# Optimization experiments

Measured on AMD Instinct MI355X. Metric: run time of the kernel, lower is better.

## Reference

```python
import jax, jax.numpy as jnp
import numpy as np

N, C_IN, H, W = 32, 256, 56, 56
C_OUT, KH, KW = 256, 3, 3
ACT_BITS = 8


def setup_inputs() -> dict:
    key = jax.random.key(0)
    k_x, k_w, k_s, k_b = jax.random.split(key, 4)
    x = jax.random.normal(k_x, (N, C_IN, H, W), dtype=jnp.float32)
    # ternary weights in {-1, 0, +1}, stored as int8
    w_q = jax.random.randint(k_w, (C_OUT, C_IN, KH, KW), -1, 2).astype(jnp.int8)
    # per-output-channel scale, broadcastable over NCHW as [C,1,1]
    s = (jax.random.uniform(k_s, (C_OUT, 1, 1), dtype=jnp.float32) * 0.02 + 0.005)
    bias = jax.random.normal(k_b, (C_OUT,), dtype=jnp.float32) * 0.1
    act_s = jnp.float32(1.0 / 127.0)  # per-tensor activation quant scale
    return {"x": x, "w_q": w_q, "s": s, "bias": bias, "act_s": act_s}


def reference(x, w_q, s, bias, act_s):
    # activation fake-quant: clamp to [-1,1], round to act_bits symmetric grid
    qmax = (1 << (ACT_BITS - 1)) - 1  # 127
    x = jnp.clip(x, -1.0, 1.0)
    x_int = jnp.clip(jnp.round(x / act_s), -qmax, qmax)
    xq = x_int * act_s
    # ternary conv (weights upcast to float), stride 1, pad 1, dilation 1
    y = jax.lax.conv_general_dilated(
        xq, w_q.astype(jnp.float32),
        window_strides=(1, 1), padding=((1, 1), (1, 1)),
        lhs_dilation=(1, 1), rhs_dilation=(1, 1),
        dimension_numbers=("NCHW", "OIHW", "NCHW"), feature_group_count=1)
    # per-output-channel scale + bias
    y = y * s + bias.reshape(1, -1, 1, 1)
    return y
```

## Files before the change

kernel.cpp:

```cpp
#include <hip/hip_runtime.h>

typedef int v4i __attribute__((ext_vector_type(4)));

#define NIMG 32
#define CIN  256
#define COUT 256
#define HW   3136
#define W56  56
#define HP   58
#define PIMG (HP * HP)
#define XQP_BYTES (NIMG * PIMG * CIN)
#define WP_BYTES  (9 * COUT * CIN)

#define BARRIER() asm volatile("s_barrier" ::: "memory")
#define VMCNT(n)  asm volatile("s_waitcnt vmcnt(" #n ")" ::: "memory")

__global__ __launch_bounds__(256) void zero_border(v4i* __restrict__ p)
{
    int i = blockIdx.x * 256 + threadIdx.x;
    if (i >= NIMG * 228 * 16) return;
    int n = i / 3648, r = i % 3648, pix = r >> 4, c = r & 15;
    int h, w;
    if (pix < 58)       { h = 0;         w = pix;       }
    else if (pix < 116) { h = 57;        w = pix - 58;  }
    else if (pix < 172) { h = pix - 115; w = 0;         }
    else                { h = pix - 171; w = 57;        }
    v4i z = {0, 0, 0, 0};
    p[(size_t)(n * PIMG + h * HP + w) * 16 + c] = z;
}

__global__ __launch_bounds__(256) void quantize_pad(
    const float* __restrict__ x, signed char* __restrict__ xqp)
{
    __shared__ int tile[64][65];
    const int n  = blockIdx.z;
    const int c0 = blockIdx.y * 64;
    const int p0 = blockIdx.x * 64;
    const int tid = threadIdx.x;

    const int px   = tid & 63;
    const int crow = tid >> 6;
    const float* xb = x + ((size_t)(n * CIN + c0)) * HW + p0;
#pragma unroll
    for (int i = 0; i < 16; ++i) {
        int c = crow + i * 4;
        float v = xb[(size_t)c * HW + px];
        v = fminf(fmaxf(v, -1.f), 1.f);
        tile[c][px] = (int)rintf(v * 127.f);
    }
    __syncthreads();

    const int c4   = tid & 15;
    const int prow = tid >> 4;
#pragma unroll
    for (int i = 0; i < 4; ++i) {
        int p  = prow + i * 16;
        int hw = p0 + p;
        int oh = hw / W56, ow = hw % W56;
        int b0 = tile[c4 * 4 + 0][p] & 255;
        int b1 = tile[c4 * 4 + 1][p] & 255;
        int b2 = tile[c4 * 4 + 2][p] & 255;
        int b3 = tile[c4 * 4 + 3][p] & 255;
        int packed = b0 | (b1 << 8) | (b2 << 16) | (b3 << 24);
        *(int*)(xqp + ((size_t)(n * PIMG + (oh + 1) * HP + (ow + 1))) * CIN
                    + c0 + c4 * 4) = packed;
    }
}

__global__ __launch_bounds__(256) void repack_w(
    const int* __restrict__ wq, signed char* __restrict__ wp2)
{
    int idx  = blockIdx.x * 256 + threadIdx.x;
    int t    = idx >> 16;
    int rem  = idx & 65535;
    int kc   = rem >> 14;
    int rem2 = rem & 16383;
    int co   = rem2 >> 6;
    int c6   = rem2 & 63;
    int ci   = kc * 64 + c6;
    wp2[idx] = (signed char)wq[(co * CIN + ci) * 9 + t];
}

__device__ __forceinline__ void gll16(const void* g, void* l)
{
    __builtin_amdgcn_global_load_lds(
        (const __attribute__((address_space(1))) int*)g,
        (__attribute__((address_space(3))) int*)l, 16, 0, 0);
}

__global__ __launch_bounds__(256) void bitconv_mfma(
    const signed char* __restrict__ xqp, const signed char* __restrict__ wp2,
    const float* __restrict__ s_, const float* __restrict__ bias,
    const float* __restrict__ act_s_p, float* __restrict__ out)
{
    __shared__ signed char lds[3][16384];

    const int tid  = threadIdx.x;
    const int lane = tid & 63;
    const int wid  = tid >> 6;
    const int wr   = wid >> 1;
    const int wc   = wid & 1;
    const int l15  = lane & 15;
    const int kg   = lane >> 4;
    const int kgs  = ((kg ^ ((l15 >> 1) & 3)) << 4);

    const int b  = blockIdx.x;
    const int w  = (b & 7) * 196 + (b >> 3);
    const int px0   = (w >> 1) * 128;
    const int cout0 = (w & 1) * 128;

    const int srow   = tid >> 2;
    const int schunk = (((tid & 3) ^ ((tid >> 3) & 3)) << 4);
    const signed char* asrc = wp2 + cout0 * 64 + srow * 64 + schunk;

    const signed char* bsrc[2];
#pragma unroll
    for (int r = 0; r < 2; ++r) {
        int p = px0 + srow + r * 64;
        int n = p / HW, q = p % HW;
        bsrc[r] = xqp
            + ((size_t)(n * PIMG + (q / W56 + 1) * HP + (q % W56 + 1))) * CIN
            + schunk;
    }

    int aoff[4], boff[4];
#pragma unroll
    for (int i = 0; i < 4; ++i)
        aoff[i] = (wr * 64 + i * 16 + l15) * 64 + kgs;
#pragma unroll
    for (int j = 0; j < 4; ++j)
        boff[j] = 8192 + (wc * 64 + j * 16 + l15) * 64 + kgs;

    v4i acc[4][4] = {};

    const int wb = wid * 1024;

    auto stage = [&](int buf, int s) {
        int t9 = s >> 2, kc = s & 3;
        int bo = ((t9 / 3 - 1) * HP + (t9 % 3 - 1)) * CIN + kc * 64;
        signed char* L = &lds[buf][0];
        const signed char* a = asrc + s * 16384;
        gll16(a,            L + wb);
        gll16(a + 4096,     L + 4096  + wb);
        gll16(bsrc[0] + bo, L + 8192  + wb);
        gll16(bsrc[1] + bo, L + 12288 + wb);
    };

    stage(0, 0);
    stage(1, 1);
    VMCNT(4);
    BARRIER();

    for (int it = 0; it < 12; ++it) {
#pragma unroll
        for (int u = 0; u < 3; ++u) {
            const int s = it * 3 + u;
            const signed char* L = &lds[u][0];

            if (s <= 33) stage((u + 2) % 3, s + 2);

            v4i a[4], bb[4];
#pragma unroll
            for (int i = 0; i < 4; ++i) a[i]  = *(const v4i*)(L + aoff[i]);
#pragma unroll
            for (int j = 0; j < 4; ++j) bb[j] = *(const v4i*)(L + boff[j]);

            BARRIER();
            __builtin_amdgcn_s_setprio(1);
#pragma unroll
            for (int i = 0; i < 2; ++i)
#pragma unroll
                for (int j = 0; j < 4; ++j)
                    acc[i][j] = __builtin_amdgcn_mfma_i32_16x16x64_i8(
                        a[i], bb[j], acc[i][j], 0, 0, 0);
            __builtin_amdgcn_s_setprio(0);

            BARRIER();
            __builtin_amdgcn_s_setprio(1);
#pragma unroll
            for (int i = 2; i < 4; ++i)
#pragma unroll
                for (int j = 0; j < 4; ++j)
                    acc[i][j] = __builtin_amdgcn_mfma_i32_16x16x64_i8(
                        a[i], bb[j], acc[i][j], 0, 0, 0);
            __builtin_amdgcn_s_setprio(0);

            if (s <= 33)      { VMCNT(4); }
            else if (s == 34) { VMCNT(0); }
            if (s < 35) BARRIER();
        }
    }

    const float a_s = act_s_p[0];
    int nn[4], hh[4];
#pragma unroll
    for (int j = 0; j < 4; ++j) {
        int op = px0 + wc * 64 + j * 16 + l15;
        nn[j] = op / HW;
        hh[j] = op % HW;
    }
#pragma unroll
    for (int i = 0; i < 4; ++i) {
        int cb = cout0 + wr * 64 + i * 16 + kg * 4;
        float sc[4], bi[4];
#pragma unroll
        for (int r = 0; r < 4; ++r) {
            sc[r] = a_s * s_[cb + r];
            bi[r] = bias[cb + r];
        }
#pragma unroll
        for (int j = 0; j < 4; ++j)
#pragma unroll
            for (int r = 0; r < 4; ++r)
                out[((size_t)(nn[j] * COUT + cb + r)) * HW + hh[j]] =
                    (float)acc[i][j][r] * sc[r] + bi[r];
    }
}

extern "C" void kernel_launch(void* const* d_in, const int* in_sizes, int n_in,
                              void* d_out, int out_size, void* d_ws, size_t ws_size,
                              hipStream_t stream)
{
    const float* x     = (const float*)d_in[0];
    const int*   w_q   = (const int*)d_in[1];
    const float* s     = (const float*)d_in[2];
    const float* bias  = (const float*)d_in[3];
    const float* act_s = (const float*)d_in[4];

    signed char* xqp = (signed char*)d_ws;
    signed char* wp2 = (signed char*)d_ws + XQP_BYTES;

    zero_border<<<(NIMG * 228 * 16 + 255) / 256, 256, 0, stream>>>((v4i*)xqp);
    quantize_pad<<<dim3(49, 4, NIMG), 256, 0, stream>>>(x, xqp);
    repack_w<<<dim3(WP_BYTES / 256), 256, 0, stream>>>(w_q, wp2);
    bitconv_mfma<<<dim3(1568), 256, 0, stream>>>(
        xqp, wp2, s, bias, act_s, (float*)d_out);
}
```

Baseline: 99.34 us.

## Enlarge conv block tile to all 256 output channels, halving grid

Each block now computes 128 pixels by all 256 output channels instead of 128x128, so activation tiles are loaded once per pixel block rather than twice. The grid drops from 1568 to 784 blocks, LDS per stage grows to 24KB, and the accumulator array doubles to 8x4. Weight and activation loads are split into separate staging calls interleaved between the two MFMA halves. This raises register pressure (launch bounds request 2 blocks per CU) and reduces the number of blocks available to spread across CUs.

```diff
diff --git a/kernel.cpp b/kernel.cpp
--- a/kernel.cpp
+++ b/kernel.cpp
@@ -88,12 +88,12 @@
         (__attribute__((address_space(3))) int*)l, 16, 0, 0);
 }
 
-__global__ __launch_bounds__(256) void bitconv_mfma(
+__global__ __launch_bounds__(256, 2) void bitconv_mfma(
     const signed char* __restrict__ xqp, const signed char* __restrict__ wp2,
     const float* __restrict__ s_, const float* __restrict__ bias,
     const float* __restrict__ act_s_p, float* __restrict__ out)
 {
-    __shared__ signed char lds[3][16384];
+    __shared__ signed char lds[3][24576];
 
     const int tid  = threadIdx.x;
     const int lane = tid & 63;
@@ -104,14 +104,12 @@
     const int kg   = lane >> 4;
     const int kgs  = ((kg ^ ((l15 >> 1) & 3)) << 4);
 
-    const int b  = blockIdx.x;
-    const int w  = (b & 7) * 196 + (b >> 3);
-    const int px0   = (w >> 1) * 128;
-    const int cout0 = (w & 1) * 128;
+    const int b   = blockIdx.x;
+    const int px0 = ((b & 7) * 98 + (b >> 3)) * 128;
 
     const int srow   = tid >> 2;
     const int schunk = (((tid & 3) ^ ((tid >> 3) & 3)) << 4);
-    const signed char* asrc = wp2 + cout0 * 64 + srow * 64 + schunk;
+    const signed char* asrc = wp2 + srow * 64 + schunk;
 
     const signed char* bsrc[2];
 #pragma unroll
@@ -123,69 +121,81 @@
             + schunk;
     }
 
-    int aoff[4], boff[4];
-#pragma unroll
-    for (int i = 0; i < 4; ++i)
-        aoff[i] = (wr * 64 + i * 16 + l15) * 64 + kgs;
+    int aoff[8], boff[4];
+#pragma unroll
+    for (int i = 0; i < 8; ++i)
+        aoff[i] = (wr * 128 + i * 16 + l15) * 64 + kgs;
 #pragma unroll
     for (int j = 0; j < 4; ++j)
-        boff[j] = 8192 + (wc * 64 + j * 16 + l15) * 64 + kgs;
-
-    v4i acc[4][4] = {};
+        boff[j] = 16384 + (wc * 64 + j * 16 + l15) * 64 + kgs;
+
+    v4i acc[8][4] = {};
 
     const int wb = wid * 1024;
 
-    auto stage = [&](int buf, int s) {
+    auto stageA = [&](int buf, int s) {
+        signed char* L = &lds[buf][0];
+        const signed char* a = asrc + s * 16384;
+#pragma unroll
+        for (int k = 0; k < 4; ++k)
+            gll16(a + k * 4096, L + k * 4096 + wb);
+    };
+    auto stageB = [&](int buf, int s) {
         int t9 = s >> 2, kc = s & 3;
         int bo = ((t9 / 3 - 1) * HP + (t9 % 3 - 1)) * CIN + kc * 64;
         signed char* L = &lds[buf][0];
-        const signed char* a = asrc + s * 16384;
-        gll16(a,            L + wb);
-        gll16(a + 4096,     L + 4096  + wb);
-        gll16(bsrc[0] + bo, L + 8192  + wb);
-        gll16(bsrc[1] + bo, L + 12288 + wb);
+        gll16(bsrc[0] + bo, L + 16384 + wb);
+        gll16(bsrc[1] + bo, L + 20480 + wb);
     };
 
-    stage(0, 0);
-    stage(1, 1);
-    VMCNT(4);
+    stageA(0, 0); stageB(0, 0);
+    stageA(1, 1); stageB(1, 1);
+    VMCNT(6);
     BARRIER();
 
     for (int it = 0; it < 12; ++it) {
 #pragma unroll
         for (int u = 0; u < 3; ++u) {
             const int s = it * 3 + u;
+            const int nb = (u + 2) % 3;
             const signed char* L = &lds[u][0];
 
-            if (s <= 33) stage((u + 2) % 3, s + 2);
-
             v4i a[4], bb[4];
 #pragma unroll
+            for (int j = 0; j < 4; ++j) bb[j] = *(const v4i*)(L + boff[j]);
+#pragma unroll
             for (int i = 0; i < 4; ++i) a[i]  = *(const v4i*)(L + aoff[i]);
-#pragma unroll
-            for (int j = 0; j < 4; ++j) bb[j] = *(const v4i*)(L + boff[j]);
+
+            if (s <= 33) stageA(nb, s + 2);
 
             BARRIER();
             __builtin_amdgcn_s_setprio(1);
 #pragma unroll
-            for (int i = 0; i < 2; ++i)
+            for (int i = 0; i < 4; ++i)
 #pragma unroll
                 for (int j = 0; j < 4; ++j)
                     acc[i][j] = __builtin_amdgcn_mfma_i32_16x16x64_i8(
                         a[i], bb[j], acc[i][j], 0, 0, 0);
             __builtin_amdgcn_s_setprio(0);
+            BARRIER();
+
+            v4i a2[4];
+#pragma unroll
+            for (int i = 0; i < 4; ++i) a2[i] = *(const v4i*)(L + aoff[4 + i]);
+
+            if (s <= 33) stageB(nb, s + 2);
 
             BARRIER();
             __builtin_amdgcn_s_setprio(1);
 #pragma unroll
-            for (int i = 2; i < 4; ++i)
+            for (int i = 0; i < 4; ++i)
 #pragma unroll
                 for (int j = 0; j < 4; ++j)
-                    acc[i][j] = __builtin_amdgcn_mfma_i32_16x16x64_i8(
-                        a[i], bb[j], acc[i][j], 0, 0, 0);
+                    acc[4 + i][j] = __builtin_amdgcn_mfma_i32_16x16x64_i8(
+                        a2[i], bb[j], acc[4 + i][j], 0, 0, 0);
             __builtin_amdgcn_s_setprio(0);
 
-            if (s <= 33)      { VMCNT(4); }
+            if (s <= 33)      { VMCNT(6); }
             else if (s == 34) { VMCNT(0); }
             if (s < 35) BARRIER();
         }
@@ -200,8 +210,8 @@
         hh[j] = op % HW;
     }
 #pragma unroll
-    for (int i = 0; i < 4; ++i) {
-        int cb = cout0 + wr * 64 + i * 16 + kg * 4;
+    for (int i = 0; i < 8; ++i) {
+        int cb = wr * 128 + i * 16 + kg * 4;
         float sc[4], bi[4];
 #pragma unroll
         for (int r = 0; r < 4; ++r) {
@@ -233,6 +243,6 @@
     zero_border<<<(NIMG * 228 * 16 + 255) / 256, 256, 0, stream>>>((v4i*)xqp);
     quantize_pad<<<dim3(49, 4, NIMG), 256, 0, stream>>>(x, xqp);
     repack_w<<<dim3(WP_BYTES / 256), 256, 0, stream>>>(w_q, wp2);
-    bitconv_mfma<<<dim3(1568), 256, 0, stream>>>(
+    bitconv_mfma<<<dim3(784), 256, 0, stream>>>(
         xqp, wp2, s, bias, act_s, (float*)d_out);
 }
```

New measurement: 98.71 us. No clear change (-0.6%).

## Load weight fragments directly to registers and quad-buffer activations in LDS

Applied to the files above, without the earlier changes.

Weight (A) tiles are no longer staged through LDS. Each wave now loads its A fragments straight from global memory into registers, with a one-step register prefetch (a_cur/a_nxt). Only the activation (B) tile goes through LDS, which now uses a 4-deep ring of 8KB buffers, and the pipeline collapses to a single barrier per K step. This is meant to cut LDS traffic and barrier count, at the cost of uncoalesced-per-wave global loads for weights, more VGPRs for the prefetched A, and redundant A reads across the two waves sharing a row.

```diff
diff --git a/kernel.cpp b/kernel.cpp
--- a/kernel.cpp
+++ b/kernel.cpp
@@ -93,7 +93,7 @@
     const float* __restrict__ s_, const float* __restrict__ bias,
     const float* __restrict__ act_s_p, float* __restrict__ out)
 {
-    __shared__ signed char lds[3][16384];
+    __shared__ signed char Bs[4][8192];
 
     const int tid  = threadIdx.x;
     const int lane = tid & 63;
@@ -111,8 +111,6 @@
 
     const int srow   = tid >> 2;
     const int schunk = (((tid & 3) ^ ((tid >> 3) & 3)) << 4);
-    const signed char* asrc = wp2 + cout0 * 64 + srow * 64 + schunk;
-
     const signed char* bsrc[2];
 #pragma unroll
     for (int r = 0; r < 2; ++r) {
@@ -123,72 +121,63 @@
             + schunk;
     }
 
-    int aoff[4], boff[4];
-#pragma unroll
-    for (int i = 0; i < 4; ++i)
-        aoff[i] = (wr * 64 + i * 16 + l15) * 64 + kgs;
+    const signed char* ap = wp2 + (cout0 + wr * 64 + l15) * 64 + kg * 16;
+
+    int boff[4];
 #pragma unroll
     for (int j = 0; j < 4; ++j)
-        boff[j] = 8192 + (wc * 64 + j * 16 + l15) * 64 + kgs;
+        boff[j] = (wc * 64 + j * 16 + l15) * 64 + kgs;
 
     v4i acc[4][4] = {};
+    v4i a_cur[4], a_nxt[4];
 
     const int wb = wid * 1024;
 
-    auto stage = [&](int buf, int s) {
+    auto stageB = [&](int buf, int s) {
         int t9 = s >> 2, kc = s & 3;
         int bo = ((t9 / 3 - 1) * HP + (t9 % 3 - 1)) * CIN + kc * 64;
-        signed char* L = &lds[buf][0];
-        const signed char* a = asrc + s * 16384;
-        gll16(a,            L + wb);
-        gll16(a + 4096,     L + 4096  + wb);
-        gll16(bsrc[0] + bo, L + 8192  + wb);
-        gll16(bsrc[1] + bo, L + 12288 + wb);
+        signed char* L = &Bs[buf][0];
+        gll16(bsrc[0] + bo, L + wb);
+        gll16(bsrc[1] + bo, L + 4096 + wb);
     };
 
-    stage(0, 0);
-    stage(1, 1);
-    VMCNT(4);
-    BARRIER();
-
-    for (int it = 0; it < 12; ++it) {
-#pragma unroll
-        for (int u = 0; u < 3; ++u) {
-            const int s = it * 3 + u;
-            const signed char* L = &lds[u][0];
-
-            if (s <= 33) stage((u + 2) % 3, s + 2);
-
-            v4i a[4], bb[4];
-#pragma unroll
-            for (int i = 0; i < 4; ++i) a[i]  = *(const v4i*)(L + aoff[i]);
-#pragma unroll
-            for (int j = 0; j < 4; ++j) bb[j] = *(const v4i*)(L + boff[j]);
-
-            BARRIER();
-            __builtin_amdgcn_s_setprio(1);
-#pragma unroll
-            for (int i = 0; i < 2; ++i)
-#pragma unroll
-                for (int j = 0; j < 4; ++j)
-                    acc[i][j] = __builtin_amdgcn_mfma_i32_16x16x64_i8(
-                        a[i], bb[j], acc[i][j], 0, 0, 0);
-            __builtin_amdgcn_s_setprio(0);
-
-            BARRIER();
-            __builtin_amdgcn_s_setprio(1);
-#pragma unroll
-            for (int i = 2; i < 4; ++i)
-#pragma unroll
-                for (int j = 0; j < 4; ++j)
-                    acc[i][j] = __builtin_amdgcn_mfma_i32_16x16x64_i8(
-                        a[i], bb[j], acc[i][j], 0, 0, 0);
-            __builtin_amdgcn_s_setprio(0);
-
-            if (s <= 33)      { VMCNT(4); }
-            else if (s == 34) { VMCNT(0); }
-            if (s < 35) BARRIER();
+    stageB(0, 0);
+    stageB(1, 1);
+#pragma unroll
+    for (int i = 0; i < 4; ++i)
+        a_cur[i] = *(const v4i*)(ap + i * 1024);
+
+    for (int s = 0; s < 36; ++s) {
+        if (s < 35) {
+            const signed char* a = ap + (s + 1) * 16384;
+#pragma unroll
+            for (int i = 0; i < 4; ++i)
+                a_nxt[i] = *(const v4i*)(a + i * 1024);
         }
+        if (s < 34) stageB((s + 2) & 3, s + 2);
+
+        if (s == 0)       { VMCNT(6); }
+        else if (s <= 33) { VMCNT(8); }
+        else if (s == 34) { VMCNT(6); }
+        else              { VMCNT(0); }
+        BARRIER();
+
+        const signed char* L = &Bs[s & 3][0];
+        v4i bb[4];
+#pragma unroll
+        for (int j = 0; j < 4; ++j) bb[j] = *(const v4i*)(L + boff[j]);
+
+        __builtin_amdgcn_s_setprio(1);
+#pragma unroll
+        for (int i = 0; i < 4; ++i)
+#pragma unroll
+            for (int j = 0; j < 4; ++j)
+                acc[i][j] = __builtin_amdgcn_mfma_i32_16x16x64_i8(
+                    a_cur[i], bb[j], acc[i][j], 0, 0, 0);
+        __builtin_amdgcn_s_setprio(0);
+
+#pragma unroll
+        for (int i = 0; i < 4; ++i) a_cur[i] = a_nxt[i];
     }
 
     const float a_s = act_s_p[0];
```

After: 115.6 us. +16.4%, slower.

## Switch to double-buffered K=128 stages with one barrier per stage

Applied to the files above, without the earlier changes.

Replaces the triple-buffered 64-wide K pipeline with a double buffer where each stage loads two K=64 slices (32KB per buffer) and waits on vmcnt(0) once per stage. The intermediate barriers between MFMA halves are removed, so each stage now has one barrier instead of three. In exchange, prefetch depth drops to a single stage ahead and each wait drains all outstanding loads, which exposes more load latency. LDS use grows from 48KB to 64KB per block, which can lower occupancy.

```diff
diff --git a/kernel.cpp b/kernel.cpp
--- a/kernel.cpp
+++ b/kernel.cpp
@@ -13,7 +13,7 @@
 #define WP_BYTES  (9 * COUT * CIN)
 
 #define BARRIER() asm volatile("s_barrier" ::: "memory")
-#define VMCNT(n)  asm volatile("s_waitcnt vmcnt(" #n ")" ::: "memory")
+#define VMCNT0()  asm volatile("s_waitcnt vmcnt(0)" ::: "memory")
 
 __global__ __launch_bounds__(256) void zero_border(v4i* __restrict__ p)
 {
@@ -88,12 +88,18 @@
         (__attribute__((address_space(3))) int*)l, 16, 0, 0);
 }
 
+__device__ __forceinline__ int boffset(int ss)
+{
+    int t9 = ss >> 2, kc = ss & 3;
+    return ((t9 / 3 - 1) * HP + (t9 % 3 - 1)) * CIN + kc * 64;
+}
+
 __global__ __launch_bounds__(256) void bitconv_mfma(
     const signed char* __restrict__ xqp, const signed char* __restrict__ wp2,
     const float* __restrict__ s_, const float* __restrict__ bias,
     const float* __restrict__ act_s_p, float* __restrict__ out)
 {
-    __shared__ signed char lds[3][16384];
+    __shared__ signed char lds[2][32768];
 
     const int tid  = threadIdx.x;
     const int lane = tid & 63;
@@ -135,29 +141,32 @@
 
     const int wb = wid * 1024;
 
-    auto stage = [&](int buf, int s) {
-        int t9 = s >> 2, kc = s & 3;
-        int bo = ((t9 / 3 - 1) * HP + (t9 % 3 - 1)) * CIN + kc * 64;
+    auto stage = [&](int buf, int t) {
         signed char* L = &lds[buf][0];
-        const signed char* a = asrc + s * 16384;
-        gll16(a,            L + wb);
-        gll16(a + 4096,     L + 4096  + wb);
-        gll16(bsrc[0] + bo, L + 8192  + wb);
-        gll16(bsrc[1] + bo, L + 12288 + wb);
+#pragma unroll
+        for (int h = 0; h < 2; ++h) {
+            const int ss = 2 * t + h;
+            const signed char* a = asrc + ss * 16384;
+            const int R = h * 16384;
+            gll16(a,        L + R + wb);
+            gll16(a + 4096, L + R + 4096 + wb);
+            int bo = boffset(ss);
+            gll16(bsrc[0] + bo, L + R + 8192  + wb);
+            gll16(bsrc[1] + bo, L + R + 12288 + wb);
+        }
     };
 
     stage(0, 0);
-    stage(1, 1);
-    VMCNT(4);
+    VMCNT0();
     BARRIER();
 
-    for (int it = 0; it < 12; ++it) {
-#pragma unroll
-        for (int u = 0; u < 3; ++u) {
-            const int s = it * 3 + u;
+    for (int it = 0; it < 9; ++it) {
+#pragma unroll
+        for (int u = 0; u < 2; ++u) {
+            const int t = it * 2 + u;
             const signed char* L = &lds[u][0];
 
-            if (s <= 33) stage((u + 2) % 3, s + 2);
+            if (t < 17) stage(u ^ 1, t + 1);
 
             v4i a[4], bb[4];
 #pragma unroll
@@ -165,29 +174,34 @@
 #pragma unroll
             for (int j = 0; j < 4; ++j) bb[j] = *(const v4i*)(L + boff[j]);
 
-            BARRIER();
             __builtin_amdgcn_s_setprio(1);
 #pragma unroll
-            for (int i = 0; i < 2; ++i)
+            for (int i = 0; i < 4; ++i)
 #pragma unroll
                 for (int j = 0; j < 4; ++j)
                     acc[i][j] = __builtin_amdgcn_mfma_i32_16x16x64_i8(
                         a[i], bb[j], acc[i][j], 0, 0, 0);
             __builtin_amdgcn_s_setprio(0);
 
-            BARRIER();
+            v4i a2[4], bb2[4];
+#pragma unroll
+            for (int i = 0; i < 4; ++i) a2[i]  = *(const v4i*)(L + 16384 + aoff[i]);
+#pragma unroll
+            for (int j = 0; j < 4; ++j) bb2[j] = *(const v4i*)(L + 16384 + boff[j]);
+
             __builtin_amdgcn_s_setprio(1);
 #pragma unroll
-            for (int i = 2; i < 4; ++i)
+            for (int i = 0; i < 4; ++i)
 #pragma unroll
                 for (int j = 0; j < 4; ++j)
                     acc[i][j] = __builtin_amdgcn_mfma_i32_16x16x64_i8(
-                        a[i], bb[j], acc[i][j], 0, 0, 0);
+                        a2[i], bb2[j], acc[i][j], 0, 0, 0);
             __builtin_amdgcn_s_setprio(0);
 
-            if (s <= 33)      { VMCNT(4); }
-            else if (s == 34) { VMCNT(0); }
-            if (s < 35) BARRIER();
+            if (t < 17) {
+                VMCNT0();
+                BARRIER();
+            }
         }
     }
 
```

Result: no change. 99.29 us (-0.0%).
